# Performance work log

Measured on AMD Instinct MI355X. Metric: run time of the kernel, lower is better.

## Reference

```python
import jax, jax.numpy as jnp
import numpy as np
from jax import lax

NUM_MASK_PARAMS = 67  # 66 weights (64 feat + 2 coord channels) + 1 bias
NUM_GEN_PARAMS = 134


def _coord_maps(h, w, dtype):
    yy = jnp.broadcast_to(jnp.linspace(-1.0, 1.0, h, dtype=dtype)[:, None], (h, w))
    xx = jnp.broadcast_to(jnp.linspace(-1.0, 1.0, w, dtype=dtype)[None, :], (h, w))
    return xx, yy


def _dynamic_head(x_cat, p):
    # x_cat: [66, H, W]; p: [num_ins, 67] -> [num_ins, H, W]
    w = p[:, :NUM_MASK_PARAMS - 1]
    b = p[:, NUM_MASK_PARAMS - 1]
    return jnp.einsum('ic,chw->ihw', w, x_cat) + b[:, None, None]


def setup_inputs() -> dict:
    key = jax.random.key(0)
    ks = jax.random.split(key, 10)
    C, HM, WM, HH, WH, MB, HID = 256, 272, 480, 136, 240, 64, 64
    rn = lambda k, s, sc=1.0: jax.random.normal(k, s, dtype=jnp.float32) * sc
    return {
        'out0': rn(ks[0], (1, C, HM, WM)),
        'out1': rn(ks[1], (1, C, HH, WH)),
        'hm_w': rn(ks[2], (1, C), 0.05),
        'hm_b': jnp.zeros((1,), jnp.float32),
        'params_w': rn(ks[3], (NUM_GEN_PARAMS, C), 0.05),
        'params_b': rn(ks[4], (NUM_GEN_PARAMS,), 0.05),
        'mb_w': rn(ks[5], (MB, C, 3, 3), 0.05),
        'mb_b': jnp.zeros((MB,), jnp.float32),
        'mlp_w1': rn(ks[6], (HM, HID), 0.05),
        'mlp_b1': jnp.zeros((HID,), jnp.float32),
        'mlp_w2': rn(ks[7], (HID, 2), 0.05),
        'mlp_b2': jnp.zeros((2,), jnp.float32),
        'num_ins': 4,
    }


def reference(out0, out1, hm_w, hm_b, params_w, params_b, mb_w, mb_b,
              mlp_w1, mlp_b1, mlp_w2, mlp_b2, num_ins):
    h_mask, w_mask = out0.shape[2], out0.shape[3]
    h_hm, w_hm = out1.shape[2], out1.shape[3]

    # ctnet head: 1x1 convs on the stride-16 feature
    hm = jnp.einsum('kc,bchw->bkhw', hm_w, out1) + hm_b[None, :, None, None]
    params = jnp.einsum('kc,bchw->bkhw', params_w, out1) + params_b[None, :, None, None]
    hm = jnp.clip(jax.nn.sigmoid(hm), 1e-4, 1.0 - 1e-4)  # [1,1,h_hm,w_hm]
    # [1,134,h,w] -> [h*w, 134]
    params_flat = jnp.transpose(params[0], (1, 2, 0)).reshape(-1, NUM_GEN_PARAMS)

    # 3x3 maxpool NMS (stride 1, pad 1), keep only local peaks
    hmax = lax.reduce_window(hm, -jnp.inf, lax.max, (1, 1, 3, 3), (1, 1, 1, 1),
                             [(0, 0), (0, 0), (1, 1), (1, 1)])
    keep = (hmax == hm).astype(hm.dtype)
    heat_nms = (hm * keep).reshape(-1)

    scores, inds = lax.top_k(heat_nms, num_ins)

    # mask branch: 3x3 conv + relu on the stride-8 feature
    mask_branch = lax.conv_general_dilated(out0, mb_w, (1, 1), 'SAME',
                                           dimension_numbers=('NCHW', 'OIHW', 'NCHW'))
    mask_branch = jax.nn.relu(mask_branch + mb_b[None, :, None, None])  # [1,64,H,W]

    xx, yy = _coord_maps(h_mask, w_mask, mask_branch.dtype)
    x_cat = jnp.concatenate([mask_branch[0], xx[None], yy[None]], axis=0)  # [66,H,W]

    gen_params = params_flat[inds]  # [num_ins, 134]
    masks0 = _dynamic_head(x_cat, gen_params[:, :NUM_MASK_PARAMS])   # [num_ins,H,W]
    regs0 = _dynamic_head(x_cat, gen_params[:, NUM_MASK_PARAMS:])    # [num_ins,H,W]

    # row-wise vertical-range MLP over h_mask
    feat_range = jnp.transpose(masks0, (0, 2, 1))  # [num_ins, w_mask, h_mask]
    h1 = jax.nn.relu(feat_range @ mlp_w1 + mlp_b1)
    feat_range = h1 @ mlp_w2 + mlp_b2  # [num_ins, w_mask, 2]

    return scores, inds, regs0, masks0, feat_range
```

## Files before the change

### kernel.cpp

```cpp
#include <hip/hip_runtime.h>
#include <math.h>
#include <limits.h>

#define C_IN 256
#define HM_H 136
#define HM_W 240
#define HM_N (HM_H * HM_W)
#define MB   64
#define MH   272
#define MW   480
#define MN   (MH * MW)
#define NP   134
#define NI   4
#define HID  64

#define REG_OFF   8
#define MASK_OFF  (8 + NI * MN)
#define FEAT_OFF  (8 + 2 * NI * MN)

#define WS_HM   0
#define WS_CV   HM_N
#define WS_CI   (HM_N + 512)
#define WS_GP   (2 * HM_N)
#define WS_WT_F 65824

typedef float  f32x4  __attribute__((ext_vector_type(4)));
typedef short  bf16x8 __attribute__((ext_vector_type(8)));
typedef unsigned short u16x8 __attribute__((ext_vector_type(8)));

__device__ __forceinline__ unsigned short f2bf(float f) {
  unsigned int u = __float_as_uint(f);
  u += 0x7FFFu + ((u >> 16) & 1u);
  return (unsigned short)(u >> 16);
}
__device__ __forceinline__ float b2f(unsigned short h) {
  return __uint_as_float(((unsigned int)h) << 16);
}

__device__ __forceinline__ void glds16(const void* g, void* l) {
  __builtin_amdgcn_global_load_lds(
      (const __attribute__((address_space(1))) unsigned int*)g,
      (__attribute__((address_space(3))) unsigned int*)l, 16, 0, 0);
}

__global__ void k_prep(const float* __restrict__ mb_w, unsigned short* __restrict__ wt,
                       const float* __restrict__ out1, const float* __restrict__ hm_w,
                       const float* __restrict__ hm_b, float* __restrict__ ws_hm) {
  __shared__ float part[4][64];
  if (blockIdx.x < 576) {
    int idx = blockIdx.x * 256 + threadIdx.x;
    int j    = idx & 7;
    int lane = (idx >> 3) & 63;
    int nt   = (idx >> 9) & 3;
    int gt   = idx >> 11;
    int t    = gt % 9;
    int g    = gt / 9;
    int n = nt * 16 + (lane & 15);
    int c = g * 32 + (lane >> 4) * 8 + j;
    wt[idx] = f2bf(mb_w[(n * C_IN + c) * 9 + t]);
  } else {
    int b = blockIdx.x - 576, t = threadIdx.x;
    int cg = t >> 6, pl = t & 63;
    int p = b * 64 + pl;
    float s = 0.f;
    #pragma unroll 16
    for (int c = 0; c < 64; ++c)
      s += hm_w[cg * 64 + c] * out1[(cg * 64 + c) * HM_N + p];
    part[cg][pl] = s;
    __syncthreads();
    if (t < 64) {
      float tot = part[0][t] + part[1][t] + part[2][t] + part[3][t] + hm_b[0];
      float sig = 1.f / (1.f + expf(-tot));
      sig = fminf(fmaxf(sig, 1e-4f), 1.f - 1e-4f);
      ws_hm[b * 64 + t] = sig;
    }
  }
}

__device__ __forceinline__ bool better(float av, int ai, float bv, int bi) {
  return (av > bv) || (av == bv && ai < bi);
}

template<int NTHR>
__device__ void top4_tree(float* sv, int* si, int t) {
  for (int s = NTHR / 2; s >= 1; s >>= 1) {
    if (t < s) {
      float a[4], b[4]; int ai[4], bj[4];
      #pragma unroll
      for (int k = 0; k < 4; ++k) {
        a[k] = sv[t * 4 + k];        ai[k] = si[t * 4 + k];
        b[k] = sv[(t + s) * 4 + k];  bj[k] = si[(t + s) * 4 + k];
      }
      float ov[4]; int oi[4];
      int i = 0, j = 0;
      #pragma unroll
      for (int k = 0; k < 4; ++k) {
        if (better(a[i], ai[i], b[j], bj[j])) { ov[k] = a[i]; oi[k] = ai[i]; ++i; }
        else                                   { ov[k] = b[j]; oi[k] = bj[j]; ++j; }
      }
      #pragma unroll
      for (int k = 0; k < 4; ++k) { sv[t * 4 + k] = ov[k]; si[t * 4 + k] = oi[k]; }
    }
    __syncthreads();
  }
}

__global__ void k_nms_top(const float* __restrict__ ws_hm, float* __restrict__ candv,
                          int* __restrict__ candi) {
  __shared__ float sv[256 * 4];
  __shared__ int   si[256 * 4];
  int b = blockIdx.x, t = threadIdx.x;
  float v = -1.f; int idx = INT_MAX;
  if (t < 255) {
    int p = b * 255 + t;
    int y = p / HM_W, x = p - y * HM_W;
    float c = ws_hm[p], m = c;
    #pragma unroll
    for (int dy = -1; dy <= 1; ++dy)
      #pragma unroll
      for (int dx = -1; dx <= 1; ++dx) {
        int yy = y + dy, xx = x + dx;
        if (yy >= 0 && yy < HM_H && xx >= 0 && xx < HM_W)
          m = fmaxf(m, ws_hm[yy * HM_W + xx]);
      }
    v = (c == m) ? c : 0.f;
    idx = p;
  }
  sv[t * 4] = v; si[t * 4] = idx;
  #pragma unroll
  for (int k = 1; k < 4; ++k) { sv[t * 4 + k] = -1.f; si[t * 4 + k] = INT_MAX; }
  __syncthreads();
  top4_tree<256>(sv, si, t);
  if (t == 0) {
    #pragma unroll
    for (int k = 0; k < 4; ++k) { candv[b * 4 + k] = sv[k]; candi[b * 4 + k] = si[k]; }
  }
}

__global__ void k_gen(const float* __restrict__ candv, const int* __restrict__ candi,
                      const float* __restrict__ out1, const float* __restrict__ params_w,
                      const float* __restrict__ params_b, float* __restrict__ ws_gp,
                      float* __restrict__ d_out) {
  __shared__ float sv[128 * 4];
  __shared__ int   si[128 * 4];
  __shared__ float col[C_IN];
  int t = threadIdx.x, i = blockIdx.x;
  if (t < 128) {
    #pragma unroll
    for (int k = 0; k < 4; ++k) { sv[t * 4 + k] = candv[t * 4 + k]; si[t * 4 + k] = candi[t * 4 + k]; }
  }
  __syncthreads();
  top4_tree<128>(sv, si, t);
  if (i == 0 && t < 4) {
    d_out[t]     = sv[t];
    d_out[4 + t] = (float)si[t];
  }
  int p = si[i];
  col[t] = out1[t * HM_N + p];
  __syncthreads();
  if (t < NP) {
    float s = params_b[t];
    #pragma unroll 8
    for (int c = 0; c < C_IN; ++c) s += params_w[t * C_IN + c] * col[c];
    ws_gp[i * NP + t] = s;
  }
}

#define SR   18
#define RP   36
#define BUFU (SR * RP * 32)
#define WOFF (2 * BUFU)

#define PIPE_BARRIER() do {                                   \
    __builtin_amdgcn_sched_barrier(0);                        \
    asm volatile("s_waitcnt lgkmcnt(0)" ::: "memory");        \
    __builtin_amdgcn_s_barrier();                             \
    __builtin_amdgcn_sched_barrier(0);                        \
  } while (0)

#define STAGE_W3(G, B)                                                    \
  if (wv == 7 && (G) < 24) {                                              \
    const char* wsrc = (const char*)wt + (G) * 12288 + lane * 16;         \
    char* wdst = (char*)smem + 2 * WOFF + (B) * 12288;                    \
    _Pragma("unroll")                                                     \
    for (int i_ = 0; i_ < 12; ++i_)                                       \
      glds16(wsrc + i_ * 1024, wdst + i_ * 1024);                         \
  }

#define MFMA16(A, B, C) __builtin_amdgcn_mfma_f32_16x16x32_bf16(A, B, C, 0, 0, 0)

#define TAPS3(P) {                                                        \
    const unsigned short* wl = smem + WOFF + (P) * 6144 + lane * 8;       \
    _Pragma("unroll")                                                     \
    for (int tt = 0; tt < 3; ++tt) {                                      \
      bf16x8 bb0 = *(const bf16x8*)(wl + tt * 2048);                      \
      bf16x8 bb1 = *(const bf16x8*)(wl + tt * 2048 + 512);                \
      bf16x8 bb2 = *(const bf16x8*)(wl + tt * 2048 + 1024);               \
      bf16x8 bb3 = *(const bf16x8*)(wl + tt * 2048 + 1536);               \
      unsigned pk = lrdp[(P) * 3 + tt];                                   \
      const unsigned short* c0 = cur + (pk & 0xFFFFu);                    \
      const unsigned short* c1 = cur + (pk >> 16);                        \
      bf16x8 a0 = *(const bf16x8*)c0;                                     \
      bf16x8 a1 = *(const bf16x8*)(c0 + 512);                             \
      bf16x8 a2 = *(const bf16x8*)c1;                                     \
      bf16x8 a3 = *(const bf16x8*)(c1 + 512);                             \
      acc[0][0] = MFMA16(a0, bb0, acc[0][0]);                             \
      acc[0][1] = MFMA16(a0, bb1, acc[0][1]);                             \
      acc[0][2] = MFMA16(a0, bb2, acc[0][2]);                             \
      acc[0][3] = MFMA16(a0, bb3, acc[0][3]);                             \
      acc[1][0] = MFMA16(a1, bb0, acc[1][0]);                             \
      acc[1][1] = MFMA16(a1, bb1, acc[1][1]);                             \
      acc[1][2] = MFMA16(a1, bb2, acc[1][2]);                             \
      acc[1][3] = MFMA16(a1, bb3, acc[1][3]);                             \
      acc[2][0] = MFMA16(a2, bb0, acc[2][0]);                             \
      acc[2][1] = MFMA16(a2, bb1, acc[2][1]);                             \
      acc[2][2] = MFMA16(a2, bb2, acc[2][2]);                             \
      acc[2][3] = MFMA16(a2, bb3, acc[2][3]);                             \
      acc[3][0] = MFMA16(a3, bb0, acc[3][0]);                             \
      acc[3][1] = MFMA16(a3, bb1, acc[3][1]);                             \
      acc[3][2] = MFMA16(a3, bb2, acc[3][2]);                             \
      acc[3][3] = MFMA16(a3, bb3, acc[3][3]);                             \
    } }

__device__ __forceinline__ void stage_store8(unsigned short* buf, const f32x4* dq,
                                             bool gv, const int* lw, unsigned sm) {
  #pragma unroll
  for (int e = 0; e < 4; ++e) if ((sm >> e) & 1u) {
    u16x8 v;
    #pragma unroll
    for (int j = 0; j < 8; ++j) v[j] = f2bf(gv ? dq[j][e] : 0.f);
    *(u16x8*)(buf + lw[e]) = v;
  }
}

__global__ __launch_bounds__(512, 2) void k_conv_mfma(
    const float* __restrict__ out0, const unsigned short* __restrict__ wt,
    const float* __restrict__ mb_b, const float* __restrict__ ws_gp,
    float* __restrict__ d_out) {
  __shared__ unsigned short smem[2 * BUFU + 3 * 6144];

  int tid  = threadIdx.x;
  int lane = tid & 63;
  int wv   = tid >> 6;
  int n15  = lane & 15;
  int kq   = lane >> 4;

  int orig = blockIdx.x;
  int xcd  = orig & 7, pos = orig >> 3;
  int wgid = (xcd < 7) ? (xcd * 32 + pos) : (224 + pos);
  int bx = wgid / 17, by = wgid - bx * 17;
  int gx0 = bx * 32, gy0 = by * 16;

  bool ustage = tid < 360;
  int u    = ustage ? tid : 0;
  int co8  = u / 180;
  int rem  = u - co8 * 180;
  int row  = rem / 10;
  int qx   = rem - row * 10;
  int iy   = gy0 + row - 1;
  int ixq  = gx0 + 4 * qx - 4;
  bool gvld = ustage && (iy >= 0) && (iy < MH) && (ixq >= 0) && (ixq + 3 < MW);
  int goffA = gvld ? (co8 * 8 * MN + iy * MW + ixq) : 0;
  int lwsA[4]; unsigned smask = 0;
  #pragma unroll
  for (int e = 0; e < 4; ++e) {
    int sx = 4 * qx - 3 + e;
    bool sv = ustage && (sx >= 0) && (sx < RP);
    int pixw = row * RP + (sv ? sx : 0);
    int w2 = (pixw ^ (pixw >> 2)) & 3;
    int q  = (pixw ^ row) & 1;
    lwsA[e] = (pixw >> 1) * 64 + ((co8 ^ w2) << 4) + q * 8;
    if (sv) smask |= (1u << e);
  }

  unsigned lrdp[9];
  #pragma unroll
  for (int t = 0; t < 9; ++t) {
    int ty = t / 3, tx = t - ty * 3;
    int sr0 = 2 * wv + ty;
    int pix0 = sr0 * RP + n15 + tx;
    int w20 = (pix0 ^ (pix0 >> 2)) & 3;
    int q0  = (pix0 ^ sr0) & 1;
    unsigned o0 = (pix0 >> 1) * 64 + ((kq ^ w20) << 4) + q0 * 8;
    int sr1 = sr0 + 1;
    int pix1 = sr1 * RP + n15 + tx;
    int w21 = (pix1 ^ (pix1 >> 2)) & 3;
    int q1  = (pix1 ^ sr1) & 1;
    unsigned o1 = (pix1 >> 1) * 64 + ((kq ^ w21) << 4) + q1 * 8;
    lrdp[t] = o0 | (o1 << 16);
  }

  f32x4 dqA[8], dqB[8];
  if (ustage) {
    const float* sp = out0 + goffA;
    #pragma unroll
    for (int j = 0; j < 8; ++j) dqA[j] = *(const f32x4*)(sp + j * MN);
  }
  stage_store8(smem, dqA, gvld, lwsA, smask);
  if (ustage) {
    const float* sp = out0 + goffA + 16 * MN;
    #pragma unroll
    for (int j = 0; j < 8; ++j) dqB[j] = *(const f32x4*)(sp + j * MN);
  }
  {
    int lwsB[4];
    #pragma unroll
    for (int e = 0; e < 4; ++e) lwsB[e] = lwsA[e] ^ 32;
    stage_store8(smem, dqB, gvld, lwsB, smask);
  }
  __builtin_amdgcn_sched_barrier(0);
  if (ustage) {
    const float* sp = out0 + 32 * MN + goffA;
    #pragma unroll
    for (int j = 0; j < 8; ++j) dqA[j] = *(const f32x4*)(sp + j * MN);
    const float* sq = out0 + 32 * MN + goffA + 16 * MN;
    #pragma unroll
    for (int j = 0; j < 8; ++j) dqB[j] = *(const f32x4*)(sq + j * MN);
  }
  __builtin_amdgcn_sched_barrier(0);
  STAGE_W3(0, 0);
  STAGE_W3(1, 1);
  if (wv == 7) asm volatile("s_waitcnt vmcnt(12)" ::: "memory");
  PIPE_BARRIER();

  f32x4 acc[4][4];
  #pragma unroll
  for (int i = 0; i < 4; ++i)
    #pragma unroll
    for (int nt = 0; nt < 4; ++nt)
      acc[i][nt] = (f32x4){0.f, 0.f, 0.f, 0.f};

  #pragma unroll 1
  for (int g = 0; g < 8; ++g) {
    const unsigned short* cur = smem + (g & 1) * BUFU;
    unsigned short*       nxt = smem + ((g + 1) & 1) * BUFU;

    STAGE_W3(3 * g + 2, 2);
    if (g < 7) stage_store8(nxt, dqA, gvld, lwsA, smask);
    __builtin_amdgcn_sched_barrier(0);
    if (g < 6 && ustage) {
      const float* sp = out0 + (g + 2) * (32 * MN) + goffA;
      #pragma unroll
      for (int j = 0; j < 8; ++j) dqA[j] = *(const f32x4*)(sp + j * MN);
    }
    __builtin_amdgcn_sched_barrier(0);
    TAPS3(0)
    if (wv == 7) asm volatile("s_waitcnt vmcnt(12)" ::: "memory");
    PIPE_BARRIER();

    STAGE_W3(3 * g + 3, 0);
    if (g < 7) {
      int lwsB[4];
      #pragma unroll
      for (int e = 0; e < 4; ++e) lwsB[e] = lwsA[e] ^ 32;
      stage_store8(nxt, dqB, gvld, lwsB, smask);
    }
    __builtin_amdgcn_sched_barrier(0);
    if (g < 6 && ustage) {
      const float* sp = out0 + (g + 2) * (32 * MN) + goffA + 16 * MN;
      #pragma unroll
      for (int j = 0; j < 8; ++j) dqB[j] = *(const f32x4*)(sp + j * MN);
    }
    __builtin_amdgcn_sched_barrier(0);
    TAPS3(1)
    if (wv == 7) {
      if (g == 7) asm volatile("s_waitcnt vmcnt(0)" ::: "memory");
      else        asm volatile("s_waitcnt vmcnt(12)" ::: "memory");
    }
    PIPE_BARRIER();

    STAGE_W3(3 * g + 4, 1);
    TAPS3(2)
    if (wv == 7) {
      if (g == 7) asm volatile("s_waitcnt vmcnt(0)" ::: "memory");
      else        asm volatile("s_waitcnt vmcnt(12)" ::: "memory");
    }
    PIPE_BARRIER();
  }

  #define ES 66
  {
    float bias[4];
    #pragma unroll
    for (int nt = 0; nt < 4; ++nt) bias[nt] = mb_b[nt * 16 + n15];
    #pragma unroll
    for (int i = 0; i < 4; ++i) {
      int pbase = (2 * wv + (i >> 1)) * 32 + (i & 1) * 16;
      #pragma unroll
      for (int nt = 0; nt < 4; ++nt)
        #pragma unroll
        for (int reg = 0; reg < 4; ++reg) {
          float vv = fmaxf(acc[i][nt][reg] + bias[nt], 0.f);
          smem[(pbase + kq * 4 + reg) * ES + nt * 16 + n15] = f2bf(vv);
        }
    }
  }
  __syncthreads();

  int p = tid & 255, hh = tid >> 8;
  int ob = hh * 32;
  float* pf = (float*)smem + 16896;
  #pragma unroll 1
  for (int ps = 0; ps < 2; ++ps) {
    int pixel = ps * 256 + p;
    float mres[4] = {0.f, 0.f, 0.f, 0.f};
    float rres[4] = {0.f, 0.f, 0.f, 0.f};
    #pragma unroll 8
    for (int o = 0; o < 32; ++o) {
      float v = b2f(smem[pixel * ES + ob + o]);
      #pragma unroll
      for (int i = 0; i < 4; ++i) {
        mres[i] += ws_gp[i * NP + ob + o] * v;
        rres[i] += ws_gp[i * NP + 67 + ob + o] * v;
      }
    }
    if (hh) {
      #pragma unroll
      for (int i = 0; i < 4; ++i) { pf[p * 8 + i] = mres[i]; pf[p * 8 + 4 + i] = rres[i]; }
    }
    __syncthreads();
    if (!hh) {
      int r = pixel >> 5, xcol = pixel & 31;
      int gy = gy0 + r, gx = gx0 + xcol;
      float xc = -1.f + (2.f / 479.f) * (float)gx;
      float yc = -1.f + (2.f / 271.f) * (float)gy;
      int pix = gy * MW + gx;
      #pragma unroll
      for (int i = 0; i < 4; ++i) {
        const float* gp = ws_gp + i * NP;
        d_out[MASK_OFF + i * MN + pix] = mres[i] + pf[p * 8 + i]     + gp[66]  + gp[64]  * xc + gp[65]  * yc;
        d_out[REG_OFF  + i * MN + pix] = rres[i] + pf[p * 8 + 4 + i] + gp[133] + gp[131] * xc + gp[132] * yc;
      }
    }
    __syncthreads();
  }
}

__global__ void k_mlp(const float* __restrict__ masks0, const float* __restrict__ w1,
                      const float* __restrict__ b1, const float* __restrict__ w2,
                      const float* __restrict__ b2, float* __restrict__ d_out) {
  int blk = blockIdx.x;
  int i = blk / MW;
  int w = blk - i * MW;
  int k = threadIdx.x;
  const float* mcol = masks0 + i * MN + w;
  float s = b1[k];
  #pragma unroll 4
  for (int h = 0; h < MH; ++h) s += mcol[h * MW] * w1[h * HID + k];
  s = fmaxf(s, 0.f);
  float o0 = s * w2[k * 2 + 0];
  float o1 = s * w2[k * 2 + 1];
  #pragma unroll
  for (int off = 32; off >= 1; off >>= 1) {
    o0 += __shfl_down(o0, off);
    o1 += __shfl_down(o1, off);
  }
  if (k == 0) {
    d_out[FEAT_OFF + blk * 2 + 0] = o0 + b2[0];
    d_out[FEAT_OFF + blk * 2 + 1] = o1 + b2[1];
  }
}

extern "C" void kernel_launch(void* const* d_in, const int* in_sizes, int n_in,
                              void* d_out, int out_size, void* d_ws, size_t ws_size,
                              hipStream_t stream) {
  const float* out0     = (const float*)d_in[0];
  const float* out1     = (const float*)d_in[1];
  const float* hm_w     = (const float*)d_in[2];
  const float* hm_b     = (const float*)d_in[3];
  const float* params_w = (const float*)d_in[4];
  const float* params_b = (const float*)d_in[5];
  const float* mb_w     = (const float*)d_in[6];
  const float* mb_b     = (const float*)d_in[7];
  const float* mlp_w1   = (const float*)d_in[8];
  const float* mlp_b1   = (const float*)d_in[9];
  const float* mlp_w2   = (const float*)d_in[10];
  const float* mlp_b2   = (const float*)d_in[11];

  float* ws      = (float*)d_ws;
  float* ws_hm   = ws + WS_HM;
  float* candv   = ws + WS_CV;
  int*   candi   = (int*)(ws + WS_CI);
  float* ws_gp   = ws + WS_GP;
  unsigned short* ws_wt = (unsigned short*)(ws + WS_WT_F);
  float* out     = (float*)d_out;

  k_prep<<<1086, 256, 0, stream>>>(mb_w, ws_wt, out1, hm_w, hm_b, ws_hm);
  k_nms_top<<<128, 256, 0, stream>>>(ws_hm, candv, candi);
  k_gen<<<NI, 256, 0, stream>>>(candv, candi, out1, params_w, params_b, ws_gp, out);
  k_conv_mfma<<<255, 512, 0, stream>>>(out0, ws_wt, mb_b, ws_gp, out);
  k_mlp<<<NI * MW, 64, 0, stream>>>(out + MASK_OFF, mlp_w1, mlp_b1, mlp_w2, mlp_b2, out);
}
```

Baseline: 307.2 us.

## Stage full per-group conv weights double-buffered and cache mask column in LDS for MLP

The conv kernel's pipeline now copies all 3 tap-weight slices of a channel group (36 KB) into a double-buffered LDS region once per group, instead of rotating a triple buffer of single-tap slices. This cuts the per-group barriers from three to one and merges the two activation stage/load phases. The cost is a larger LDS footprint, which may limit the two-blocks-per-CU occupancy, and coarser-grained overlap, since the weight wait is vmcnt(0) at the end of each group. Separately, the MLP kernel loads each mask column into shared memory once, so the strided global reads are no longer repeated by every thread.

```diff
diff --git a/kernel.cpp b/kernel.cpp
--- a/kernel.cpp
+++ b/kernel.cpp
@@ -169,7 +169,8 @@
 #define SR   18
 #define RP   36
 #define BUFU (SR * RP * 32)
-#define WOFF (2 * BUFU)
+#define WBASE (2 * BUFU)
+#define WBUFU 18432
 
 #define PIPE_BARRIER() do {                                   \
     __builtin_amdgcn_sched_barrier(0);                        \
@@ -178,19 +179,20 @@
     __builtin_amdgcn_sched_barrier(0);                        \
   } while (0)
 
-#define STAGE_W3(G, B)                                                    \
-  if (wv == 7 && (G) < 24) {                                              \
-    const char* wsrc = (const char*)wt + (G) * 12288 + lane * 16;         \
-    char* wdst = (char*)smem + 2 * WOFF + (B) * 12288;                    \
+#define STAGE_W_ALL(G)                                                    \
+  if (wv == 7 && (G) < 8) {                                               \
+    const char* wsrc = (const char*)wt + (G) * 36864 + lane * 16;         \
+    char* wdst = (char*)smem + 82944 + ((G) & 1) * 36864;                 \
     _Pragma("unroll")                                                     \
-    for (int i_ = 0; i_ < 12; ++i_)                                       \
+    for (int i_ = 0; i_ < 36; ++i_)                                       \
       glds16(wsrc + i_ * 1024, wdst + i_ * 1024);                         \
   }
 
 #define MFMA16(A, B, C) __builtin_amdgcn_mfma_f32_16x16x32_bf16(A, B, C, 0, 0, 0)
 
 #define TAPS3(P) {                                                        \
-    const unsigned short* wl = smem + WOFF + (P) * 6144 + lane * 8;       \
+    const unsigned short* wl = smem + WBASE + ((g) & 1) * WBUFU           \
+                               + (P) * 6144 + lane * 8;                   \
     _Pragma("unroll")                                                     \
     for (int tt = 0; tt < 3; ++tt) {                                      \
       bf16x8 bb0 = *(const bf16x8*)(wl + tt * 2048);                      \
@@ -237,7 +239,7 @@
     const float* __restrict__ out0, const unsigned short* __restrict__ wt,
     const float* __restrict__ mb_b, const float* __restrict__ ws_gp,
     float* __restrict__ d_out) {
-  __shared__ unsigned short smem[2 * BUFU + 3 * 6144];
+  __shared__ unsigned short smem[2 * BUFU + 2 * WBUFU];
 
   int tid  = threadIdx.x;
   int lane = tid & 63;
@@ -318,9 +320,8 @@
     for (int j = 0; j < 8; ++j) dqB[j] = *(const f32x4*)(sq + j * MN);
   }
   __builtin_amdgcn_sched_barrier(0);
-  STAGE_W3(0, 0);
-  STAGE_W3(1, 1);
-  if (wv == 7) asm volatile("s_waitcnt vmcnt(12)" ::: "memory");
+  STAGE_W_ALL(0);
+  if (wv == 7) asm volatile("s_waitcnt vmcnt(0)" ::: "memory");
   PIPE_BARRIER();
 
   f32x4 acc[4][4];
@@ -335,46 +336,30 @@
     const unsigned short* cur = smem + (g & 1) * BUFU;
     unsigned short*       nxt = smem + ((g + 1) & 1) * BUFU;
 
-    STAGE_W3(3 * g + 2, 2);
-    if (g < 7) stage_store8(nxt, dqA, gvld, lwsA, smask);
+    STAGE_W_ALL(g + 1);
+    if (g < 7) {
+      stage_store8(nxt, dqA, gvld, lwsA, smask);
+      int lwsB[4];
+      #pragma unroll
+      for (int e = 0; e < 4; ++e) lwsB[e] = lwsA[e] ^ 32;
+      stage_store8(nxt, dqB, gvld, lwsB, smask);
+    }
     __builtin_amdgcn_sched_barrier(0);
     if (g < 6 && ustage) {
       const float* sp = out0 + (g + 2) * (32 * MN) + goffA;
       #pragma unroll
       for (int j = 0; j < 8; ++j) dqA[j] = *(const f32x4*)(sp + j * MN);
+      const float* sq = out0 + (g + 2) * (32 * MN) + goffA + 16 * MN;
+      #pragma unroll
+      for (int j = 0; j < 8; ++j) dqB[j] = *(const f32x4*)(sq + j * MN);
     }
     __builtin_amdgcn_sched_barrier(0);
+
     TAPS3(0)
-    if (wv == 7) asm volatile("s_waitcnt vmcnt(12)" ::: "memory");
-    PIPE_BARRIER();
-
-    STAGE_W3(3 * g + 3, 0);
-    if (g < 7) {
-      int lwsB[4];
-      #pragma unroll
-      for (int e = 0; e < 4; ++e) lwsB[e] = lwsA[e] ^ 32;
-      stage_store8(nxt, dqB, gvld, lwsB, smask);
-    }
-    __builtin_amdgcn_sched_barrier(0);
-    if (g < 6 && ustage) {
-      const float* sp = out0 + (g + 2) * (32 * MN) + goffA + 16 * MN;
-      #pragma unroll
-      for (int j = 0; j < 8; ++j) dqB[j] = *(const f32x4*)(sp + j * MN);
-    }
-    __builtin_amdgcn_sched_barrier(0);
     TAPS3(1)
-    if (wv == 7) {
-      if (g == 7) asm volatile("s_waitcnt vmcnt(0)" ::: "memory");
-      else        asm volatile("s_waitcnt vmcnt(12)" ::: "memory");
-    }
-    PIPE_BARRIER();
-
-    STAGE_W3(3 * g + 4, 1);
     TAPS3(2)
-    if (wv == 7) {
-      if (g == 7) asm volatile("s_waitcnt vmcnt(0)" ::: "memory");
-      else        asm volatile("s_waitcnt vmcnt(12)" ::: "memory");
-    }
+
+    if (wv == 7) asm volatile("s_waitcnt vmcnt(0)" ::: "memory");
     PIPE_BARRIER();
   }
 
@@ -439,14 +424,17 @@
 __global__ void k_mlp(const float* __restrict__ masks0, const float* __restrict__ w1,
                       const float* __restrict__ b1, const float* __restrict__ w2,
                       const float* __restrict__ b2, float* __restrict__ d_out) {
+  __shared__ float ms[MH];
   int blk = blockIdx.x;
   int i = blk / MW;
   int w = blk - i * MW;
   int k = threadIdx.x;
   const float* mcol = masks0 + i * MN + w;
+  for (int h = k; h < MH; h += 64) ms[h] = mcol[h * MW];
+  __syncthreads();
   float s = b1[k];
-  #pragma unroll 4
-  for (int h = 0; h < MH; ++h) s += mcol[h * MW] * w1[h * HID + k];
+  #pragma unroll 8
+  for (int h = 0; h < MH; ++h) s += ms[h] * w1[h * HID + k];
   s = fmaxf(s, 0.f);
   float o0 = s * w2[k * 2 + 0];
   float o1 = s * w2[k * 2 + 1];
```

Measured after the change: 297.7 us. 1.03x faster.
